# Kernel optimization log

Hardware: AMD Instinct MI355X
Metric: run time of the kernel (lower is better)

Reference implementation:

```python
import jax, jax.numpy as jnp
import numpy as np

ALPHA, BETA, LAMDA = 0.4, 2.0, 2.0
N_VIEWS, BATCH, DIM = 12, 4096, 128


def setup_inputs() -> dict:
    key = jax.random.key(0)
    k1, k2, k3, k4 = jax.random.split(key, 4)
    return {
        "SV_A": jax.random.normal(k1, (N_VIEWS, BATCH, DIM), dtype=jnp.float32),
        "SV_N": jax.random.normal(k2, (N_VIEWS, BATCH, DIM), dtype=jnp.float32),
        "MV_A": jax.random.normal(k3, (BATCH, DIM), dtype=jnp.float32),
        "MV_N": jax.random.normal(k4, (BATCH, DIM), dtype=jnp.float32),
    }


def reference(SV_A, SV_N, MV_A, MV_N):
    # expanded pairwise SQUARED distances across views, per batch element
    diff = SV_A[:, None, :, :] - SV_N[None, :, :, :]      # [nA, nN, B, D]
    d = jnp.sum(diff * diff, axis=-1)                     # [nA, nN, B]
    nA, nN, B = d.shape

    # hard-negative (confuser) mining: globally closest cross-object view pair per sample
    idx = jnp.argmin(d.reshape(nA * nN, B), axis=0)       # [B]
    conf_A = idx // nN
    conf_N = idx % nN
    b = jnp.arange(B)
    f_conf_A = SV_A[conf_A, b, :]                         # [B, D]
    f_conf_N = SV_N[conf_N, b, :]                         # [B, D]

    # inter-class distance between MV embeddings (euclidean, matches torch.cdist)
    mv_inter = jnp.sqrt(jnp.sum((MV_A - MV_N) ** 2, axis=-1))   # [B]
    # inter-class distance between confuser embeddings (squared, matches min of d)
    mc_inter = jnp.min(d, axis=(0, 1))                           # [B]
    # intra-class distances MV <-> confuser (euclidean)
    a_clstr = jnp.sqrt(jnp.sum((MV_A - f_conf_A) ** 2, axis=-1))  # [B]
    c_intra = jnp.sqrt(jnp.sum((MV_N - f_conf_N) ** 2, axis=-1))  # [B]

    loss_m_cluster = jax.nn.relu(a_clstr - ALPHA)
    loss_c_cluster = jax.nn.relu(c_intra - ALPHA)
    loss_mc_inter = jax.nn.relu(BETA - mc_inter)
    loss_mv_inter = jax.nn.relu(BETA - mv_inter)

    losses = LAMDA * (loss_mc_inter + loss_mv_inter) + loss_m_cluster + loss_c_cluster

    info_quads = [
        jnp.count_nonzero(losses),
        jnp.mean(jnp.sqrt(mc_inter)),
        0.5 * (jnp.mean(jnp.sqrt(a_clstr)) + jnp.mean(jnp.sqrt(c_intra))),
        jnp.min(jnp.sqrt(mc_inter)),
    ]
    avg_loss = jnp.mean(losses)
    return avg_loss, info_quads
```

## Files before the change

kernel.cpp:

```cpp
#include <hip/hip_runtime.h>
#include <math.h>

#define NV 12
#define BATCH 4096
#define DIM 128
#define ALPHA_C 0.4f
#define BETA_C 2.0f
#define LAMDA_C 2.0f
#define LDSPAD 132
#define BPB 4

__device__ __forceinline__ void acc4(const float4 a, const float4 n, float& s) {
    float dx;
    dx = a.x - n.x; s += dx * dx;
    dx = a.y - n.y; s += dx * dx;
    dx = a.z - n.z; s += dx * dx;
    dx = a.w - n.w; s += dx * dx;
}

__global__ __launch_bounds__(256) void perb_kernel(
    const float* __restrict__ SV_A, const float* __restrict__ SV_N,
    const float* __restrict__ MV_A, const float* __restrict__ MV_N,
    float4* __restrict__ perb)
{
    const int wave = threadIdx.x >> 6;
    const int lane = threadIdx.x & 63;
    const int b    = blockIdx.x * BPB + wave;

    __shared__ float As[BPB][NV][LDSPAD];
    __shared__ float Ns[BPB][NV][LDSPAD];

    {
        const int half = lane >> 5;
        const int c    = (lane & 31) * 4;
        #pragma unroll
        for (int r = 0; r < NV / 2; ++r) {
            const int i = 2 * r + half;
            const size_t off = ((size_t)(i * BATCH + b)) * DIM + c;
            *(float4*)&As[wave][i][c] = *(const float4*)(SV_A + off);
            *(float4*)&Ns[wave][i][c] = *(const float4*)(SV_N + off);
        }
    }

    float best_d = 3.4e38f;
    int   best_p = 1 << 20;
    if (lane < 36) {
        const int i2 = lane / 6;
        const int j2 = lane % 6;
        const float* a0p = As[wave][2 * i2];
        const float* a1p = As[wave][2 * i2 + 1];
        const float* n0p = Ns[wave][2 * j2];
        const float* n1p = Ns[wave][2 * j2 + 1];
        float s00 = 0.f, s01 = 0.f, s10 = 0.f, s11 = 0.f;
        #pragma unroll
        for (int k = 0; k < DIM; k += 4) {
            const float4 a0 = *(const float4*)(a0p + k);
            const float4 a1 = *(const float4*)(a1p + k);
            const float4 n0 = *(const float4*)(n0p + k);
            const float4 n1 = *(const float4*)(n1p + k);
            acc4(a0, n0, s00);
            acc4(a0, n1, s01);
            acc4(a1, n0, s10);
            acc4(a1, n1, s11);
        }
        const int p00 = (2 * i2) * NV + 2 * j2;
        best_d = s00; best_p = p00;
        if (s01 < best_d) { best_d = s01; best_p = p00 + 1; }
        if (s10 < best_d) { best_d = s10; best_p = p00 + NV; }
        if (s11 < best_d) { best_d = s11; best_p = p00 + NV + 1; }
    }

    #pragma unroll
    for (int off = 32; off > 0; off >>= 1) {
        const float od = __shfl_down(best_d, off, 64);
        const int   op = __shfl_down(best_p, off, 64);
        if (od < best_d || (od == best_d && op < best_p)) { best_d = od; best_p = op; }
    }
    best_d = __shfl(best_d, 0, 64);
    best_p = __shfl(best_p, 0, 64);

    const int istar = best_p / NV;
    const int jstar = best_p % NV;

    float sa = 0.f, sc = 0.f, sm = 0.f;
    #pragma unroll
    for (int t = 0; t < 2; ++t) {
        const int k = lane + t * 64;
        const float ma = MV_A[(size_t)b * DIM + k];
        const float mn = MV_N[(size_t)b * DIM + k];
        const float fa = As[wave][istar][k];
        const float fn = Ns[wave][jstar][k];
        float d1;
        d1 = ma - fa; sa += d1 * d1;
        d1 = mn - fn; sc += d1 * d1;
        d1 = ma - mn; sm += d1 * d1;
    }
    #pragma unroll
    for (int off = 32; off > 0; off >>= 1) {
        sa += __shfl_down(sa, off, 64);
        sc += __shfl_down(sc, off, 64);
        sm += __shfl_down(sm, off, 64);
    }

    if (lane == 0) {
        const float mc    = best_d;
        const float a_cl  = sqrtf(sa);
        const float c_in  = sqrtf(sc);
        const float mv_in = sqrtf(sm);
        const float loss  = LAMDA_C * (fmaxf(BETA_C - mc, 0.f) + fmaxf(BETA_C - mv_in, 0.f))
                          + fmaxf(a_cl - ALPHA_C, 0.f) + fmaxf(c_in - ALPHA_C, 0.f);
        float4 o;
        o.x = loss;
        o.y = (loss != 0.f) ? 1.f : 0.f;
        o.z = sqrtf(mc);
        o.w = 0.5f * (sqrtf(a_cl) + sqrtf(c_in));
        perb[b] = o;
    }
}

__global__ __launch_bounds__(1024) void final_kernel(
    const float4* __restrict__ perb, float* __restrict__ out)
{
    const int t = threadIdx.x;
    float sl = 0.f, sn = 0.f, ss = 0.f, sh = 0.f, mnv = 3.4e38f;
    #pragma unroll
    for (int u = 0; u < BATCH / 1024; ++u) {
        const float4 v = perb[t + u * 1024];
        sl += v.x; sn += v.y; ss += v.z; sh += v.w;
        mnv = fminf(mnv, v.z);
    }
    #pragma unroll
    for (int off = 32; off > 0; off >>= 1) {
        sl += __shfl_down(sl, off, 64);
        sn += __shfl_down(sn, off, 64);
        ss += __shfl_down(ss, off, 64);
        sh += __shfl_down(sh, off, 64);
        mnv = fminf(mnv, __shfl_down(mnv, off, 64));
    }
    __shared__ float r[16][5];
    const int w = t >> 6;
    if ((t & 63) == 0) {
        r[w][0] = sl; r[w][1] = sn; r[w][2] = ss; r[w][3] = sh; r[w][4] = mnv;
    }
    __syncthreads();
    if (t == 0) {
        #pragma unroll
        for (int i = 1; i < 16; ++i) {
            sl += r[i][0]; sn += r[i][1]; ss += r[i][2]; sh += r[i][3];
            mnv = fminf(mnv, r[i][4]);
        }
        const float inv = 1.0f / (float)BATCH;
        out[0] = sl * inv;
        out[1] = sn;
        out[2] = ss * inv;
        out[3] = sh * inv;
        out[4] = mnv;
    }
}

extern "C" void kernel_launch(void* const* d_in, const int* in_sizes, int n_in,
                              void* d_out, int out_size, void* d_ws, size_t ws_size,
                              hipStream_t stream) {
    const float* SV_A = (const float*)d_in[0];
    const float* SV_N = (const float*)d_in[1];
    const float* MV_A = (const float*)d_in[2];
    const float* MV_N = (const float*)d_in[3];
    float* out = (float*)d_out;
    float4* perb = (float4*)d_ws;

    perb_kernel<<<BATCH / BPB, 256, 0, stream>>>(SV_A, SV_N, MV_A, MV_N, perb);
    final_kernel<<<1, 1024, 0, stream>>>(perb, out);
}
```

Measured before the change: 99.75 us.

## Compute pairwise distances via norm expansion and prefetch MV rows early

Replaces the direct squared-difference accumulation with the ||a||^2+||n||^2-2a·n expansion. Row norms are precomputed once per view in LDS, so the inner loop becomes pure FMAs instead of subtract-plus-FMA. MV_A/MV_N loads are also hoisted to the kernel start so they overlap with the SV loads. This adds a norm pass and an extra LDS read phase without a barrier between waves. The expansion can change argmin tie-breaking and the precision of the minimum distance.

```diff
diff --git a/kernel.cpp b/kernel.cpp
--- a/kernel.cpp
+++ b/kernel.cpp
@@ -10,14 +10,6 @@
 #define LDSPAD 132
 #define BPB 4
 
-__device__ __forceinline__ void acc4(const float4 a, const float4 n, float& s) {
-    float dx;
-    dx = a.x - n.x; s += dx * dx;
-    dx = a.y - n.y; s += dx * dx;
-    dx = a.z - n.z; s += dx * dx;
-    dx = a.w - n.w; s += dx * dx;
-}
-
 __global__ __launch_bounds__(256) void perb_kernel(
     const float* __restrict__ SV_A, const float* __restrict__ SV_N,
     const float* __restrict__ MV_A, const float* __restrict__ MV_N,
@@ -29,6 +21,14 @@
 
     __shared__ float As[BPB][NV][LDSPAD];
     __shared__ float Ns[BPB][NV][LDSPAD];
+    __shared__ float normsA[BPB][NV];
+    __shared__ float normsN[BPB][NV];
+
+    const size_t mvoff = (size_t)b * DIM + lane;
+    const float ma0 = MV_A[mvoff];
+    const float ma1 = MV_A[mvoff + 64];
+    const float mn0 = MV_N[mvoff];
+    const float mn1 = MV_N[mvoff + 64];
 
     {
         const int half = lane >> 5;
@@ -40,6 +40,20 @@
             *(float4*)&As[wave][i][c] = *(const float4*)(SV_A + off);
             *(float4*)&Ns[wave][i][c] = *(const float4*)(SV_N + off);
         }
+    }
+
+    if (lane < 2 * NV) {
+        const int arr = lane >= NV;
+        const int row = arr ? (lane - NV) : lane;
+        const float* p = arr ? Ns[wave][row] : As[wave][row];
+        float nrm = 0.f;
+        #pragma unroll
+        for (int k = 0; k < DIM; k += 4) {
+            const float4 v = *(const float4*)(p + k);
+            nrm += v.x * v.x + v.y * v.y + v.z * v.z + v.w * v.w;
+        }
+        if (arr) normsN[wave][row] = nrm;
+        else     normsA[wave][row] = nrm;
     }
 
     float best_d = 3.4e38f;
@@ -58,16 +72,24 @@
             const float4 a1 = *(const float4*)(a1p + k);
             const float4 n0 = *(const float4*)(n0p + k);
             const float4 n1 = *(const float4*)(n1p + k);
-            acc4(a0, n0, s00);
-            acc4(a0, n1, s01);
-            acc4(a1, n0, s10);
-            acc4(a1, n1, s11);
+            s00 += a0.x * n0.x + a0.y * n0.y + a0.z * n0.z + a0.w * n0.w;
+            s01 += a0.x * n1.x + a0.y * n1.y + a0.z * n1.z + a0.w * n1.w;
+            s10 += a1.x * n0.x + a1.y * n0.y + a1.z * n0.z + a1.w * n0.w;
+            s11 += a1.x * n1.x + a1.y * n1.y + a1.z * n1.z + a1.w * n1.w;
         }
+        const float na0 = normsA[wave][2 * i2];
+        const float na1 = normsA[wave][2 * i2 + 1];
+        const float nn0 = normsN[wave][2 * j2];
+        const float nn1 = normsN[wave][2 * j2 + 1];
+        const float d00 = na0 + nn0 - 2.f * s00;
+        const float d01 = na0 + nn1 - 2.f * s01;
+        const float d10 = na1 + nn0 - 2.f * s10;
+        const float d11 = na1 + nn1 - 2.f * s11;
         const int p00 = (2 * i2) * NV + 2 * j2;
-        best_d = s00; best_p = p00;
-        if (s01 < best_d) { best_d = s01; best_p = p00 + 1; }
-        if (s10 < best_d) { best_d = s10; best_p = p00 + NV; }
-        if (s11 < best_d) { best_d = s11; best_p = p00 + NV + 1; }
+        best_d = d00; best_p = p00;
+        if (d01 < best_d) { best_d = d01; best_p = p00 + 1; }
+        if (d10 < best_d) { best_d = d10; best_p = p00 + NV; }
+        if (d11 < best_d) { best_d = d11; best_p = p00 + NV + 1; }
     }
 
     #pragma unroll
@@ -82,18 +104,19 @@
     const int istar = best_p / NV;
     const int jstar = best_p % NV;
 
-    float sa = 0.f, sc = 0.f, sm = 0.f;
-    #pragma unroll
-    for (int t = 0; t < 2; ++t) {
-        const int k = lane + t * 64;
-        const float ma = MV_A[(size_t)b * DIM + k];
-        const float mn = MV_N[(size_t)b * DIM + k];
-        const float fa = As[wave][istar][k];
-        const float fn = Ns[wave][jstar][k];
+    float sa, sc, sm;
+    {
+        const float fa0 = As[wave][istar][lane];
+        const float fa1 = As[wave][istar][lane + 64];
+        const float fn0 = Ns[wave][jstar][lane];
+        const float fn1 = Ns[wave][jstar][lane + 64];
         float d1;
-        d1 = ma - fa; sa += d1 * d1;
-        d1 = mn - fn; sc += d1 * d1;
-        d1 = ma - mn; sm += d1 * d1;
+        d1 = ma0 - fa0; sa  = d1 * d1;
+        d1 = ma1 - fa1; sa += d1 * d1;
+        d1 = mn0 - fn0; sc  = d1 * d1;
+        d1 = mn1 - fn1; sc += d1 * d1;
+        d1 = ma0 - mn0; sm  = d1 * d1;
+        d1 = ma1 - mn1; sm += d1 * d1;
     }
     #pragma unroll
     for (int off = 32; off > 0; off >>= 1) {
@@ -103,7 +126,7 @@
     }
 
     if (lane == 0) {
-        const float mc    = best_d;
+        const float mc    = fmaxf(best_d, 0.f);
         const float a_cl  = sqrtf(sa);
         const float c_in  = sqrtf(sc);
         const float mv_in = sqrtf(sm);
```

New measurement: 99.53 us. No clear change (-0.2%).
